# Optimization experiments

Hardware: AMD Instinct MI355X
Metric: run time of the kernel (lower is better)

The kernel has to match this reference:

```python
import jax, jax.numpy as jnp
import numpy as np

B, C, T = 32, 512, 1024
SIG_LO, SIG_HI = 1.0, 10.0   # sigma_range
THR, BETA = 0.5, 0.95        # snn.Leaky(beta=0.95, threshold=thr)
KSIZE = 13


def setup_inputs() -> dict:
    key = jax.random.key(0)
    inp = jax.random.normal(key, (B, 1, C, T), dtype=jnp.float32)
    # nn.Parameter initialized to sigma_range.mean() = 5.5
    w = jnp.float32((SIG_LO + SIG_HI) / 2.0)
    return {"inp": inp, "w": w}


def _gaussian_kernel(sigma):
    # matches gaussian_kernel(size=13): linspace(-6, 6, 13), normalized
    r = jnp.linspace(-(KSIZE // 2), KSIZE // 2, KSIZE).astype(jnp.float32)
    k = jnp.exp(-0.5 * (r / sigma) ** 2)
    return k / k.sum()


def _atan_spike(u):
    # snntorch default ATan surrogate (alpha=2): fwd heaviside, bwd 1/(1+(pi*u)^2)
    soft = jnp.arctan(jnp.pi * u) / jnp.pi
    hard = (u > 0).astype(u.dtype)
    return soft + jax.lax.stop_gradient(hard - soft)


def reference(inp, w):
    x = inp[:, 0]  # (B, C, T)
    # w_eff = sigma_range.mean() + clamp(w, 1, 10); identical for every sample,
    # so the per-sample/per-timestep kernels of the original are all equal.
    sigma = (SIG_LO + SIG_HI) / 2.0 + jnp.clip(w, SIG_LO, SIG_HI)
    k = _gaussian_kernel(sigma)  # (13,)
    # 13-tap Gaussian smoothing along the channel axis, all timesteps at once
    x_mean = jax.lax.conv_general_dilated(
        x[:, None],                    # (B,1,C,T)
        k[None, None, :, None],        # (1,1,13,1)
        window_strides=(1, 1),
        padding=((KSIZE // 2, KSIZE // 2), (0, 0)),
        dimension_numbers=("NCHW", "OIHW", "NCHW"),
    )[:, 0]                            # (B,C,T)
    drive = jnp.transpose(x - x_mean, (2, 0, 1))  # (T,B,C)

    def step(mem, xt):
        # snntorch Leaky, reset_mechanism='subtract'; reset is detached
        reset = jax.lax.stop_gradient((mem > THR).astype(mem.dtype))
        mem = BETA * mem + xt - reset * THR
        spk = _atan_spike(mem - THR)
        return mem, spk

    mem0 = jnp.zeros((B, C), dtype=jnp.float32)
    _, spks = jax.lax.scan(step, mem0, drive)  # (T,B,C)
    return jnp.transpose(spks, (1, 2, 0))[:, None]  # (B,1,C,T)
```

## Files before the change

### kernel.cpp

```cpp
#include <hip/hip_runtime.h>
#include <math.h>

constexpr int Bn = 32;
constexpr int Cn = 512;
constexpr int Tn = 1024;
constexpr int KS = 13;

constexpr int CB   = 64;
constexpr int TT   = 64;
constexpr int NCH  = Tn / TT;
constexpr int DSTR = TT + 1;
constexpr int NL   = 34;

__global__ __launch_bounds__(256, 1)
void snn_fused(const float* __restrict__ x, const float* __restrict__ wp,
               float* __restrict__ out) {
  __shared__ float D[2][CB][DSTR];
  __shared__ float S[CB][DSTR];

  const int tid = threadIdx.x;
  const int b   = blockIdx.y;
  const int c0  = blockIdx.x * CB;
  const long xbase = (long)b * Cn * Tn;

  float kw[KS];
  {
    float w  = wp[0];
    float wc = fminf(fmaxf(w, 1.0f), 10.0f);
    float sigma = __fadd_rn(5.5f, wc);
    float e[KS];
#pragma unroll
    for (int i = 0; i < KS; ++i) {
      float q = __fdiv_rn((float)(i - 6), sigma);
      float t = __fmul_rn(-0.5f, __fmul_rn(q, q));
      e[i] = (float)exp((double)t);
    }
    float s = __fadd_rn(
        __fadd_rn(__fadd_rn(e[0], e[1]), __fadd_rn(e[2], e[3])),
        __fadd_rn(__fadd_rn(e[4], e[5]), __fadd_rn(e[6], e[7])));
    s = __fadd_rn(s, e[8]);  s = __fadd_rn(s, e[9]);  s = __fadd_rn(s, e[10]);
    s = __fadd_rn(s, e[11]); s = __fadd_rn(s, e[12]);
#pragma unroll
    for (int i = 0; i < KS; ++i) kw[i] = __fdiv_rn(e[i], s);
  }

  const bool convw = (tid >= 64);
  const int  tl    = tid & 63;
  const int  segS  = convw ? ((tid >> 6) - 1) * 21 : 0;
  const int  cin0  = c0 + segS - 6;

  float xp[NL], xn[NL];

  auto load_chunk = [&](int m, float* dst) {
#pragma unroll
    for (int j = 0; j < NL; ++j) {
      const int gc = cin0 + j;
      float v = 0.0f;
      if (gc >= 0 && gc < Cn)
        v = x[xbase + (long)gc * Tn + m * TT + tl];
      dst[j] = v;
    }
  };
  auto conv_chunk = [&](int parity) {
#pragma unroll
    for (int r = 0; r < 22; ++r) {
      float acc = __fmul_rn(kw[0], xp[r]);
#pragma unroll
      for (int i = 1; i < KS; ++i)
        acc = __fadd_rn(acc, __fmul_rn(kw[i], xp[r + i]));
      D[parity][segS + r][tl] = __fsub_rn(xp[r + 6], acc);
    }
  };

  if (convw) {
    load_chunk(0, xp);
    load_chunk(1, xn);
    conv_chunk(0);
#pragma unroll
    for (int j = 0; j < NL; ++j) xp[j] = xn[j];
  }
  __syncthreads();

  float mem = 0.0f;

  for (int k = 0; k < NCH; ++k) {
    if (!convw) {
      if (k > 0) {
        const int t0p = (k - 1) * TT;
#pragma unroll 8
        for (int r = 0; r < CB; ++r)
          out[xbase + (long)(c0 + r) * Tn + t0p + tl] = S[r][tl];
      }
      const int c = tl;
      float (*Dc)[DSTR] = D[k & 1];
      for (int tt = 0; tt < TT; tt += 8) {
        float dv[8];
#pragma unroll
        for (int j = 0; j < 8; ++j) dv[j] = Dc[c][tt + j];
#pragma unroll
        for (int j = 0; j < 8; ++j) {
          const float rthr = (mem > 0.5f) ? 0.5f : 0.0f;
          float a  = __fmul_rn(0.95f, mem);
          float s2 = __fadd_rn(a, dv[j]);
          mem = __fsub_rn(s2, rthr);
          S[c][tt + j] = (mem > 0.5f) ? 1.0f : 0.0f;
        }
      }
    } else {
      if (k + 2 < NCH) load_chunk(k + 2, xn);
      if (k + 1 < NCH) {
        conv_chunk((k + 1) & 1);
#pragma unroll
        for (int j = 0; j < NL; ++j) xp[j] = xn[j];
      }
    }
    __syncthreads();
  }

  if (!convw) {
    const int t0p = (NCH - 1) * TT;
#pragma unroll 8
    for (int r = 0; r < CB; ++r)
      out[xbase + (long)(c0 + r) * Tn + t0p + tl] = S[r][tl];
  }
}

extern "C" void kernel_launch(void* const* d_in, const int* in_sizes, int n_in,
                              void* d_out, int out_size, void* d_ws, size_t ws_size,
                              hipStream_t stream) {
  const float* x  = (const float*)d_in[0];
  const float* w  = (const float*)d_in[1];
  float* out      = (float*)d_out;
  dim3 grid(Cn / CB, Bn, 1);
  snn_fused<<<grid, 256, 0, stream>>>(x, w, out);
}
```

Measured before the change: 133.3 us.

## Offload spike stores to conv warps, bit-pack spikes, widen conv split

Raises the block to 576 threads: one 64-thread scan wave plus eight conv waves of 8 channels each, replacing three waves of 21-22 channels. The scan wave now packs its 64 spikes per channel into a 64-bit mask in shared memory and no longer writes to global memory. The conv waves expand the masks and store the output, which takes the global writes off the serial scan's critical path. Register ping-pong between two load buffers replaces the per-chunk array copy. The cost is more threads per block and a larger relative halo overhead per conv segment.

```diff
diff --git a/kernel.cpp b/kernel.cpp
--- a/kernel.cpp
+++ b/kernel.cpp
@@ -10,13 +10,15 @@
 constexpr int TT   = 64;
 constexpr int NCH  = Tn / TT;
 constexpr int DSTR = TT + 1;
-constexpr int NL   = 34;
+constexpr int NSEG = 8;
+constexpr int SEG  = CB / NSEG;
+constexpr int NL   = SEG + KS - 1;
 
-__global__ __launch_bounds__(256, 1)
+__global__ __launch_bounds__(576, 1)
 void snn_fused(const float* __restrict__ x, const float* __restrict__ wp,
                float* __restrict__ out) {
   __shared__ float D[2][CB][DSTR];
-  __shared__ float S[CB][DSTR];
+  __shared__ unsigned long long Sb[2][CB];
 
   const int tid = threadIdx.x;
   const int b   = blockIdx.y;
@@ -44,12 +46,14 @@
     for (int i = 0; i < KS; ++i) kw[i] = __fdiv_rn(e[i], s);
   }
 
-  const bool convw = (tid >= 64);
-  const int  tl    = tid & 63;
-  const int  segS  = convw ? ((tid >> 6) - 1) * 21 : 0;
+  const bool scanw = (tid < 64);
+  const int  ctid  = tid - 64;
+  const int  col   = ctid & 63;
+  const int  cseg  = ctid >> 6;
+  const int  segS  = cseg * SEG;
   const int  cin0  = c0 + segS - 6;
 
-  float xp[NL], xn[NL];
+  float xA[NL], xB[NL];
 
   auto load_chunk = [&](int m, float* dst) {
 #pragma unroll
@@ -57,72 +61,78 @@
       const int gc = cin0 + j;
       float v = 0.0f;
       if (gc >= 0 && gc < Cn)
-        v = x[xbase + (long)gc * Tn + m * TT + tl];
+        v = x[xbase + (long)gc * Tn + m * TT + col];
       dst[j] = v;
     }
   };
-  auto conv_chunk = [&](int parity) {
+  auto conv_chunk = [&](const float* xs, int p) {
 #pragma unroll
-    for (int r = 0; r < 22; ++r) {
-      float acc = __fmul_rn(kw[0], xp[r]);
+    for (int r = 0; r < SEG; ++r) {
+      float acc = __fmul_rn(kw[0], xs[r]);
 #pragma unroll
       for (int i = 1; i < KS; ++i)
-        acc = __fadd_rn(acc, __fmul_rn(kw[i], xp[r + i]));
-      D[parity][segS + r][tl] = __fsub_rn(xp[r + 6], acc);
+        acc = __fadd_rn(acc, __fmul_rn(kw[i], xs[r + i]));
+      D[p][segS + r][col] = __fsub_rn(xs[r + 6], acc);
+    }
+  };
+  auto store_spikes = [&](int m) {
+    const int t0p = m * TT;
+#pragma unroll
+    for (int r = 0; r < SEG; ++r) {
+      const unsigned long long wb = Sb[m & 1][segS + r];
+      const float v = ((wb >> col) & 1ull) ? 1.0f : 0.0f;
+      out[xbase + (long)(c0 + segS + r) * Tn + t0p + col] = v;
     }
   };
 
-  if (convw) {
-    load_chunk(0, xp);
-    load_chunk(1, xn);
-    conv_chunk(0);
-#pragma unroll
-    for (int j = 0; j < NL; ++j) xp[j] = xn[j];
+  if (!scanw) {
+    load_chunk(0, xA);
+    load_chunk(1, xB);
+    conv_chunk(xA, 0);
   }
   __syncthreads();
 
   float mem = 0.0f;
 
   for (int k = 0; k < NCH; ++k) {
-    if (!convw) {
-      if (k > 0) {
-        const int t0p = (k - 1) * TT;
-#pragma unroll 8
-        for (int r = 0; r < CB; ++r)
-          out[xbase + (long)(c0 + r) * Tn + t0p + tl] = S[r][tl];
-      }
-      const int c = tl;
+    if (scanw) {
+      const int c = tid;
       float (*Dc)[DSTR] = D[k & 1];
-      for (int tt = 0; tt < TT; tt += 8) {
-        float dv[8];
+      unsigned int lo = 0u, hi = 0u;
+      float dvA[16], dvB[16];
 #pragma unroll
-        for (int j = 0; j < 8; ++j) dv[j] = Dc[c][tt + j];
+      for (int j = 0; j < 16; ++j) dvA[j] = Dc[c][j];
 #pragma unroll
-        for (int j = 0; j < 8; ++j) {
+      for (int g = 0; g < 4; ++g) {
+        const float* cur = (g & 1) ? dvB : dvA;
+        float*       nxt = (g & 1) ? dvA : dvB;
+        if (g < 3) {
+#pragma unroll
+          for (int j = 0; j < 16; ++j) nxt[j] = Dc[c][(g + 1) * 16 + j];
+        }
+#pragma unroll
+        for (int j = 0; j < 16; ++j) {
+          const int t = g * 16 + j;
           const float rthr = (mem > 0.5f) ? 0.5f : 0.0f;
           float a  = __fmul_rn(0.95f, mem);
-          float s2 = __fadd_rn(a, dv[j]);
+          float s2 = __fadd_rn(a, cur[j]);
           mem = __fsub_rn(s2, rthr);
-          S[c][tt + j] = (mem > 0.5f) ? 1.0f : 0.0f;
+          const unsigned int bit = (mem > 0.5f) ? 1u : 0u;
+          if (t < 32) lo |= bit << t;
+          else        hi |= bit << (t - 32);
         }
       }
+      Sb[k & 1][c] = ((unsigned long long)hi << 32) | (unsigned long long)lo;
     } else {
-      if (k + 2 < NCH) load_chunk(k + 2, xn);
-      if (k + 1 < NCH) {
-        conv_chunk((k + 1) & 1);
-#pragma unroll
-        for (int j = 0; j < NL; ++j) xp[j] = xn[j];
-      }
+      const bool even = ((k & 1) == 0);
+      if (k + 2 < NCH) { if (even) load_chunk(k + 2, xA); else load_chunk(k + 2, xB); }
+      if (k > 0) store_spikes(k - 1);
+      if (k + 1 < NCH) { if (even) conv_chunk(xB, (k + 1) & 1); else conv_chunk(xA, (k + 1) & 1); }
     }
     __syncthreads();
   }
 
-  if (!convw) {
-    const int t0p = (NCH - 1) * TT;
-#pragma unroll 8
-    for (int r = 0; r < CB; ++r)
-      out[xbase + (long)(c0 + r) * Tn + t0p + tl] = S[r][tl];
-  }
+  if (!scanw) store_spikes(NCH - 1);
 }
 
 extern "C" void kernel_launch(void* const* d_in, const int* in_sizes, int n_in,
@@ -132,5 +142,5 @@
   const float* w  = (const float*)d_in[1];
   float* out      = (float*)d_out;
   dim3 grid(Cn / CB, Bn, 1);
-  snn_fused<<<grid, 256, 0, stream>>>(x, w, out);
+  snn_fused<<<grid, 576, 0, stream>>>(x, w, out);
 }
```

Result: slower. 222.3 us (+66.7%).
